# Kernel tuning notes

Measured on AMD Instinct MI355X. Metric: run time of the kernel, lower is better.

Reference implementation:

```python
import jax, jax.numpy as jnp
import numpy as np

L, D, B, N, H = 18, 256, 2, 1024, 4
HD = D // H  # head dim = 64
NAMES = ['self', 'cross'] * 9
BN_EPS = 1e-5


def conv1d(x, W, b):
    # pointwise Conv1d: x [B, Cin, N], W [Cout, Cin], b [Cout]
    return jnp.einsum('oi,bin->bon', W, x) + b[None, :, None]


def setup_inputs() -> dict:
    key = jax.random.key(0)
    ks = jax.random.split(key, 20)
    r = lambda k, shp, s=0.02: jax.random.normal(k, shp, dtype=jnp.float32) * s
    inp = {
        'desc0': jax.random.normal(ks[0], (B, D, N), dtype=jnp.float32),
        'desc1': jax.random.normal(ks[1], (B, D, N), dtype=jnp.float32),
        # attention projections (q, k, v, merge), stacked over layers
        'Wq': r(ks[2], (L, D, D)), 'bq': r(ks[3], (L, D)),
        'Wk': r(ks[4], (L, D, D)), 'bk': r(ks[5], (L, D)),
        'Wv': r(ks[6], (L, D, D)), 'bv': r(ks[7], (L, D)),
        'Wm': r(ks[8], (L, D, D)), 'bm': r(ks[9], (L, D)),
        # MLP([2D, 2D, D]): conv1 + BN(eval) + relu + conv2
        'W1': r(ks[10], (L, 2 * D, 2 * D)), 'b1': r(ks[11], (L, 2 * D)),
        'gamma': 1.0 + r(ks[12], (L, 2 * D)), 'beta': r(ks[13], (L, 2 * D)),
        'mu': r(ks[14], (L, 2 * D), 0.1),
        'var': 0.5 + jax.random.uniform(ks[15], (L, 2 * D), dtype=jnp.float32),
        'W2': r(ks[16], (L, D, 2 * D)), 'b2': r(ks[17], (L, D)),
    }
    return inp


def reference(desc0, desc1, Wq, bq, Wk, bk, Wv, bv, Wm, bm,
              W1, b1, gamma, beta, mu, var, W2, b2):
    d0, d1 = desc0, desc1
    bs = d0.shape[0]
    out0, out1 = [], []
    for i, name in enumerate(NAMES):
        x = jnp.concatenate([d0, d1], axis=0)           # [2B, D, N]
        src = x if name == 'self' else jnp.concatenate([d1, d0], axis=0)
        # QKV projections, split D -> (head_dim, H) matching torch .view(B, dim, H, -1)
        q = conv1d(x, Wq[i], bq[i]).reshape(2 * bs, HD, H, N)
        k = conv1d(src, Wk[i], bk[i]).reshape(2 * bs, HD, H, N)
        v = conv1d(src, Wv[i], bv[i]).reshape(2 * bs, HD, H, N)
        scores = jnp.einsum('bdhn,bdhm->bhnm', q, k) / np.sqrt(HD).astype(np.float32)
        prob = jax.nn.softmax(scores, axis=-1)          # [2B, H, N, N]
        att = jnp.einsum('bhnm,bdhm->bdhn', prob, v).reshape(2 * bs, D, N)
        message = conv1d(att, Wm[i], bm[i])             # merge
        y = jnp.concatenate([x, message], axis=1)       # [2B, 2D, N]
        h = conv1d(y, W1[i], b1[i])
        h = gamma[i][None, :, None] * (h - mu[i][None, :, None]) \
            * jax.lax.rsqrt(var[i][None, :, None] + BN_EPS) + beta[i][None, :, None]
        h = jax.nn.relu(h)
        delta = conv1d(h, W2[i], b2[i])                 # [2B, D, N]
        d0 = d0 + delta[:bs]
        d1 = d1 + delta[bs:]
        if name == 'cross':
            out0.append(d0)
            out1.append(d1)
    # [2, n_cross, B, D, N]
    return jnp.stack([jnp.stack(out0), jnp.stack(out1)])
```

## Files before the change

### kernel.cpp

```cpp
#include <hip/hip_runtime.h>
#include <math.h>


typedef unsigned short u16;
typedef unsigned int u32;
typedef __attribute__((ext_vector_type(4))) unsigned int u32x4;
typedef __attribute__((ext_vector_type(2))) unsigned int u32x2;
typedef __attribute__((ext_vector_type(8))) short short8v;
typedef __attribute__((ext_vector_type(4))) float f32x4;

union AB { u32x4 q; u32x2 d[2]; short8v s; };

__device__ __forceinline__ u16 f2bf(float f) {
  u32 u = __builtin_bit_cast(u32, f);
  u32 r = u + 0x7fffu + ((u >> 16) & 1u);
  return (u16)(r >> 16);
}

typedef const __attribute__((address_space(1))) void gas_t;
typedef __attribute__((address_space(3))) void las_t;
__device__ __forceinline__ void gld16(const void* g, void* l) {
  __builtin_amdgcn_global_load_lds((gas_t*)g, (las_t*)l, 16, 0, 0);
}
template<int NN>
__device__ __forceinline__ void waitvm() {
  if constexpr (NN == 0) asm volatile("s_waitcnt vmcnt(0)" ::: "memory");
  else if constexpr (NN == 1) asm volatile("s_waitcnt vmcnt(1)" ::: "memory");
  else if constexpr (NN == 2) asm volatile("s_waitcnt vmcnt(2)" ::: "memory");
  else if constexpr (NN == 3) asm volatile("s_waitcnt vmcnt(3)" ::: "memory");
  else asm volatile("s_waitcnt vmcnt(4)" ::: "memory");
}

template<int SN, int NK>
__device__ __forceinline__ void mm16g(const u16* __restrict__ Ar,
                                      const u16* const (&Br)[SN], f32x4 (&acc)[SN]) {
#pragma unroll
  for (int s = 0; s < SN; ++s) acc[s] = (f32x4){0.f, 0.f, 0.f, 0.f};
  AB a[2], b[2][SN];
  a[0].q = *(const u32x4*)(Ar);
#pragma unroll
  for (int s = 0; s < SN; ++s) b[0][s].q = *(const u32x4*)(Br[s]);
#pragma unroll
  for (int kp = 0; kp < NK; ++kp) {
    const int cu = kp & 1, nx = cu ^ 1;
    if (kp + 1 < NK) {
      a[nx].q = *(const u32x4*)(Ar + (kp + 1) * 32);
#pragma unroll
      for (int s = 0; s < SN; ++s) b[nx][s].q = *(const u32x4*)(Br[s] + (kp + 1) * 32);
    }
#pragma unroll
    for (int s = 0; s < SN; ++s)
      acc[s] = __builtin_amdgcn_mfma_f32_16x16x32_bf16(a[cu].s, b[cu][s].s, acc[s], 0, 0, 0);
  }
}

template<int LDB, int SN, int NS, int D>
__device__ __forceinline__ void mmlds(const u16* __restrict__ W, char* __restrict__ Wb,
                                      const char* __restrict__ Alds, f32x4 (&acc)[SN],
                                      int w, int lane, int l4, int l15, int R) {
  constexpr int NBUF = D + 1;
  constexpr int WREG = NBUF * SN * 1024;
  const int xj = (lane & 3) ^ ((lane >> 2) & 3) ^ ((lane >> 4) & 3);
  const int swzr = ((l15 & 3) ^ ((l15 >> 2) & 3)) << 4;
  const u16* gs = W + (size_t)(w * SN * 16 + (lane >> 2)) * LDB + xj * 8;
  char* ldsw = Wb + w * WREG;
#pragma unroll
  for (int s = 0; s < SN; ++s) acc[s] = (f32x4){0.f, 0.f, 0.f, 0.f};
#pragma unroll
  for (int d = 0; d < D; ++d) {
    const int sl = (R + d) & (NS - 1);
#pragma unroll
    for (int c = 0; c < SN; ++c)
      gld16(gs + (size_t)c * 16 * LDB + (size_t)sl * 32,
            ldsw + d * (SN * 1024) + c * 1024);
  }
#pragma unroll
  for (int i = 0; i < NS; ++i) {
    const int rem = NS - 1 - i;
    constexpr int DM1 = D - 1;
    if (rem >= DM1) waitvm<SN * DM1>();
    else if (rem == 2) waitvm<SN * 2>();
    else if (rem == 1) waitvm<SN>();
    else waitvm<0>();
    const int s = (i + R) & (NS - 1);
    const char* rb = ldsw + (i % NBUF) * (SN * 1024);
    AB af;
    af.q = *(const u32x4*)(Alds + ((l15 * 1024 + s * 64 + l4 * 16) ^ ((l15 & 7) << 4)));
#pragma unroll
    for (int t = 0; t < SN; ++t) {
      AB bf;
      bf.q = *(const u32x4*)(rb + t * 1024 + l15 * 64 + ((l4 << 4) ^ swzr));
      acc[t] = __builtin_amdgcn_mfma_f32_16x16x32_bf16(af.s, bf.s, acc[t], 0, 0, 0);
    }
    if (i + D < NS) {
      const int sl = (i + D + R) & (NS - 1);
#pragma unroll
      for (int c = 0; c < SN; ++c)
        gld16(gs + (size_t)c * 16 * LDB + (size_t)sl * 32,
              ldsw + ((i + D) % NBUF) * (SN * 1024) + c * 1024);
    }
  }
}

__global__ void k_setup(const float* __restrict__ Wq, const float* __restrict__ Wk,
                        const float* __restrict__ Wv, const float* __restrict__ Wm,
                        const float* __restrict__ W1, const float* __restrict__ W2,
                        const float* __restrict__ g, const float* __restrict__ be,
                        const float* __restrict__ mu, const float* __restrict__ va,
                        const float* __restrict__ b1, u16* __restrict__ wbf,
                        float* __restrict__ sc, float* __restrict__ sh) {
  int bid = blockIdx.x, tid = threadIdx.x;
  if (bid < 4608) {
    int which = bid / 1152, lb = bid - which * 1152;
    size_t i4 = ((size_t)lb * 256 + tid) * 4;
    int layer = (int)(i4 >> 16), rem = (int)(i4 & 65535);
    int row = rem >> 8, kk = rem & 255;
    const float* src = which == 0 ? Wq : which == 1 ? Wk : which == 2 ? Wv : Wm;
    f32x4 a = *(const f32x4*)(src + i4);
    u16* dl = wbf + (size_t)layer * 655360 + which * 65536;
    if (which < 3) {
      float s = (which == 0) ? 0.125f : 1.0f;
      int rp = ((row & 3) << 6) | (row >> 2);
      u32x2 pk;
      pk[0] = (u32)f2bf(a[0] * s) | ((u32)f2bf(a[1] * s) << 16);
      pk[1] = (u32)f2bf(a[2] * s) | ((u32)f2bf(a[3] * s) << 16);
      *(u32x2*)(dl + rp * 256 + kk) = pk;
    } else {
#pragma unroll
      for (int e = 0; e < 4; ++e) {
        int ci = kk + e, cp = ((ci & 3) << 6) | (ci >> 2);
        dl[row * 256 + cp] = f2bf(a[e]);
      }
    }
  } else if (bid < 9216) {
    int lb = bid - 4608;
    size_t i4 = ((size_t)lb * 256 + tid) * 4;
    int layer = (int)(i4 >> 18);
    size_t rem = i4 & 262143;
    f32x4 a = *(const f32x4*)(W1 + i4);
    u32x2 pk;
    pk[0] = (u32)f2bf(a[0]) | ((u32)f2bf(a[1]) << 16);
    pk[1] = (u32)f2bf(a[2]) | ((u32)f2bf(a[3]) << 16);
    *(u32x2*)(wbf + (size_t)layer * 655360 + 262144 + rem) = pk;
  } else if (bid < 11520) {
    int lb = bid - 9216;
    size_t i4 = ((size_t)lb * 256 + tid) * 4;
    int layer = (int)(i4 >> 17);
    size_t rem = i4 & 131071;
    f32x4 a = *(const f32x4*)(W2 + i4);
    u32x2 pk;
    pk[0] = (u32)f2bf(a[0]) | ((u32)f2bf(a[1]) << 16);
    pk[1] = (u32)f2bf(a[2]) | ((u32)f2bf(a[3]) << 16);
    *(u32x2*)(wbf + (size_t)layer * 655360 + 524288 + rem) = pk;
  } else {
    int i = (bid - 11520) * 256 + tid;
    if (i < 9216) {
      float s = g[i] * rsqrtf(va[i] + 1e-5f);
      sc[i] = s;
      sh[i] = s * (b1[i] - mu[i]) + be[i];
    }
  }
}

__global__ __launch_bounds__(256) void k_init(const float* __restrict__ d0,
                                              const float* __restrict__ d1,
                                              float* __restrict__ dstate,
                                              u16* __restrict__ y) {
  __shared__ float T[64 * 65];
  int b = blockIdx.z, cb = blockIdx.y * 64, nb = blockIdx.x * 64;
  int t = threadIdx.x, th = t >> 4, tl = t & 15;
  const float* src = (b < 2 ? d0 : d1) + (size_t)(b & 1) * 262144;
#pragma unroll
  for (int it = 0; it < 4; ++it) {
    int cl = it * 16 + th;
    f32x4 v = *(const f32x4*)(src + (size_t)(cb + cl) * 1024 + nb + tl * 4);
#pragma unroll
    for (int e = 0; e < 4; ++e) T[cl * 65 + tl * 4 + e] = v[e];
  }
  __syncthreads();
#pragma unroll
  for (int it = 0; it < 4; ++it) {
    int nl = it * 16 + th;
    f32x4 o;
#pragma unroll
    for (int e = 0; e < 4; ++e) o[e] = T[(tl * 4 + e) * 65 + nl];
    *(f32x4*)(dstate + (size_t)b * 262144 + (size_t)(nb + nl) * 256 + cb + tl * 4) = o;
    u32x2 pk;
    pk[0] = (u32)f2bf(o[0]) | ((u32)f2bf(o[1]) << 16);
    pk[1] = (u32)f2bf(o[2]) | ((u32)f2bf(o[3]) << 16);
    *(u32x2*)(y + (size_t)b * 524288 + (size_t)(nb + nl) * 512 + cb + tl * 4) = pk;
  }
}

__global__ __launch_bounds__(512) void k_qkv0(const u16* __restrict__ y,
                                              const u16* __restrict__ wln,
                                              const float* __restrict__ bqn,
                                              const float* __restrict__ bkn,
                                              const float* __restrict__ bvn,
                                              u16* __restrict__ qb, u16* __restrict__ kb,
                                              u16* __restrict__ vb) {
  const int row0 = blockIdx.x * 16, b = row0 >> 10, nb0 = row0 & 1023;
  const int tid = threadIdx.x, w = tid >> 6, lane = tid & 63;
  const int l4 = lane >> 4, l15 = lane & 15;
  const u16* Ar = y + (size_t)(row0 + l15) * 512 + l4 * 8;
  const u16* Br[6];
  f32x4 acc[6];
  int ty[6], cc[6];
#pragma unroll
  for (int s = 0; s < 6; ++s) {
    int gc = w * 96 + s * 16;
    ty[s] = gc >> 8;
    cc[s] = gc & 255;
    Br[s] = wln + ty[s] * 65536 + (size_t)(cc[s] + l15) * 256 + l4 * 8;
  }
  mm16g<6, 8>(Ar, Br, acc);
#pragma unroll
  for (int s = 0; s < 6; ++s) {
    int c = cc[s] + l15;
    int borig = ((c & 63) << 2) | (c >> 6);
    if (ty[s] == 0) {
      float bb = 0.125f * bqn[borig];
#pragma unroll
      for (int r = 0; r < 4; ++r)
        qb[(size_t)b * 262144 + (size_t)(nb0 + l4 * 4 + r) * 256 + c] = f2bf(acc[s][r] + bb);
    } else if (ty[s] == 1) {
      float bb = bkn[borig];
#pragma unroll
      for (int r = 0; r < 4; ++r)
        kb[(size_t)b * 262144 + (size_t)(nb0 + l4 * 4 + r) * 256 + c] = f2bf(acc[s][r] + bb);
    } else {
      float bb = bvn[borig];
      u32x2 pk;
      pk[0] = (u32)f2bf(acc[s][0] + bb) | ((u32)f2bf(acc[s][1] + bb) << 16);
      pk[1] = (u32)f2bf(acc[s][2] + bb) | ((u32)f2bf(acc[s][3] + bb) << 16);
      *(u32x2*)(vb + (size_t)b * 262144 + (size_t)c * 1024 + nb0 + l4 * 4) = pk;
    }
  }
}

__global__ __launch_bounds__(512) void k_attn(const u16* __restrict__ qbuf,
                                              const u16* __restrict__ kbuf,
                                              const u16* __restrict__ vbuf,
                                              u16* __restrict__ att, int crossmask) {
  __shared__ char Kt[2][2][8192];
  __shared__ char Vt[2][2][8192];
  __shared__ char Ps[8][2304];
  __shared__ float Ms[4][16], Ls[4][16], Os[4][16][68];
  const int nb = blockIdx.x * 64;
  const int bh = blockIdx.y, b = bh >> 2, h = bh & 3;
  const int srcb = b ^ crossmask;
  const int tid = threadIdx.x, w = tid >> 6, lane = tid & 63;
  const int l4 = lane >> 4, l15 = lane & 15;
  const int qt = w & 3, half = w >> 2;
  char* P = Ps[w];
  const u16* Qb = qbuf + (size_t)b * 262144 + h * 64;
  const u16* Kb = kbuf + (size_t)srcb * 262144 + h * 64;
  const u16* Vb = vbuf + (size_t)srcb * 262144 + (size_t)h * 65536;
  const int srow = tid >> 3, sj = (tid & 7) * 16, sx = sj ^ ((srow & 7) << 4);
  const u16* gK[2] = {Kb, Kb + 512 * 256};
  const u16* gV[2] = {Vb, Vb + 512};

  const int qrow = nb + qt * 16;
  AB qf[2];
#pragma unroll
  for (int ks = 0; ks < 2; ++ks)
    qf[ks].q = *(const u32x4*)(Qb + (size_t)(qrow + l15) * 256 + ks * 32 + l4 * 8);

  u32x4 sk[2], sv[2];
#pragma unroll
  for (int H = 0; H < 2; ++H) {
    sk[H] = *(const u32x4*)((const char*)(gK[H] + (size_t)srow * 256) + sj);
    sv[H] = *(const u32x4*)((const char*)(gV[H] + (size_t)srow * 1024) + sj);
  }
#pragma unroll
  for (int H = 0; H < 2; ++H) {
    *(u32x4*)(Kt[H][0] + srow * 128 + sx) = sk[H];
    *(u32x4*)(Vt[H][0] + srow * 128 + sx) = sv[H];
  }
  __syncthreads();

  f32x4 oacc[4];
#pragma unroll
  for (int s = 0; s < 4; ++s) oacc[s] = (f32x4){0.f, 0.f, 0.f, 0.f};
  float mst = -1e30f, lst = 0.f;

#pragma unroll
  for (int mt = 0; mt < 8; ++mt) {
    const int cur = mt & 1, nx = cur ^ 1;
    if (mt < 7) {
#pragma unroll
      for (int H = 0; H < 2; ++H) {
        sk[H] = *(const u32x4*)((const char*)(gK[H] + (size_t)((mt + 1) * 64 + srow) * 256) + sj);
        sv[H] = *(const u32x4*)((const char*)(gV[H] + (size_t)srow * 1024 + (mt + 1) * 64) + sj);
      }
    }
    f32x4 sa[4];
#pragma unroll
    for (int sm = 0; sm < 4; ++sm) {
      sa[sm] = (f32x4){0.f, 0.f, 0.f, 0.f};
#pragma unroll
      for (int ks = 0; ks < 2; ++ks) {
        AB kf;
        int rr = sm * 16 + l15;
        kf.q = *(const u32x4*)(Kt[half][cur] + rr * 128 + ((ks * 64 + l4 * 16) ^ ((rr & 7) << 4)));
        sa[sm] = __builtin_amdgcn_mfma_f32_16x16x32_bf16(kf.s, qf[ks].s, sa[sm], 0, 0, 0);
      }
    }
    float m1 = fmaxf(fmaxf(fmaxf(sa[0][0], sa[0][1]), fmaxf(sa[0][2], sa[0][3])),
                     fmaxf(fmaxf(sa[1][0], sa[1][1]), fmaxf(sa[1][2], sa[1][3])));
    float m2 = fmaxf(fmaxf(fmaxf(sa[2][0], sa[2][1]), fmaxf(sa[2][2], sa[2][3])),
                     fmaxf(fmaxf(sa[3][0], sa[3][1]), fmaxf(sa[3][2], sa[3][3])));
    m1 = fmaxf(m1, m2);
    m1 = fmaxf(m1, __shfl_xor(m1, 16));
    m1 = fmaxf(m1, __shfl_xor(m1, 32));
    float mnew = fmaxf(mst, m1);
    float corr = __expf(mst - mnew);
    mst = mnew;
    float rs = 0.f;
#pragma unroll
    for (int sm = 0; sm < 4; ++sm)
#pragma unroll
      for (int r = 0; r < 4; ++r) {
        float p = __expf(sa[sm][r] - mnew);
        sa[sm][r] = p;
        rs += p;
      }
    rs += __shfl_xor(rs, 16);
    rs += __shfl_xor(rs, 32);
    lst = lst * corr + rs;
#pragma unroll
    for (int r = 0; r < 4; ++r) {
      float cr = __shfl(corr, l4 * 4 + r);
#pragma unroll
      for (int s = 0; s < 4; ++s) oacc[s][r] *= cr;
    }
#pragma unroll
    for (int sm = 0; sm < 4; ++sm) {
      u32x2 pk;
      pk[0] = (u32)f2bf(sa[sm][0]) | ((u32)f2bf(sa[sm][1]) << 16);
      pk[1] = (u32)f2bf(sa[sm][2]) | ((u32)f2bf(sa[sm][3]) << 16);
      *(u32x2*)(P + l15 * 136 + (sm * 16 + l4 * 4) * 2) = pk;
    }
#pragma unroll
    for (int ks = 0; ks < 2; ++ks) {
      AB pf;
      const char* ra = P + l15 * 136 + ks * 64 + l4 * 16;
      pf.d[0] = *(const u32x2*)ra;
      pf.d[1] = *(const u32x2*)(ra + 8);
#pragma unroll
      for (int s = 0; s < 4; ++s) {
        AB vf;
        int rr = s * 16 + l15;
        vf.q = *(const u32x4*)(Vt[half][cur] + rr * 128 + ((ks * 64 + l4 * 16) ^ ((rr & 7) << 4)));
        oacc[s] = __builtin_amdgcn_mfma_f32_16x16x32_bf16(pf.s, vf.s, oacc[s], 0, 0, 0);
      }
    }
    if (mt < 7) {
#pragma unroll
      for (int H = 0; H < 2; ++H) {
        *(u32x4*)(Kt[H][nx] + srow * 128 + sx) = sk[H];
        *(u32x4*)(Vt[H][nx] + srow * 128 + sx) = sv[H];
      }
    }
    __syncthreads();
  }
  if (half == 1) {
    Ms[qt][l15] = mst;
    Ls[qt][l15] = lst;
#pragma unroll
    for (int s = 0; s < 4; ++s)
#pragma unroll
      for (int r = 0; r < 4; ++r) Os[qt][l4 * 4 + r][s * 16 + l15] = oacc[s][r];
  }
  __syncthreads();
  if (half == 0) {
    float mb = Ms[qt][l15], lb = Ls[qt][l15];
    float M = fmaxf(mst, mb);
    float ea = __expf(mst - M), eb = __expf(mb - M);
    float rl = 1.f / (lst * ea + lb * eb);
    float fa = ea * rl, fb = eb * rl;
#pragma unroll
    for (int r = 0; r < 4; ++r) {
      float far = __shfl(fa, l4 * 4 + r);
      float fbr = __shfl(fb, l4 * 4 + r);
      int n = nb + qt * 16 + l4 * 4 + r;
#pragma unroll
      for (int s = 0; s < 4; ++s) {
        float ov = oacc[s][r] * far + Os[qt][l4 * 4 + r][s * 16 + l15] * fbr;
        att[(size_t)b * 262144 + (size_t)n * 256 + h * 64 + s * 16 + l15] = f2bf(ov);
      }
    }
  }
}

__global__ __launch_bounds__(1024) void k_post(
    const u16* __restrict__ att, const u16* __restrict__ wl, const u16* __restrict__ wln,
    const float* __restrict__ bm, const float* __restrict__ sc, const float* __restrict__ sh,
    const float* __restrict__ b2, const float* __restrict__ bqn,
    const float* __restrict__ bkn, const float* __restrict__ bvn,
    float* __restrict__ dstate, u16* __restrict__ y, u16* __restrict__ qb,
    u16* __restrict__ kb, u16* __restrict__ vb, float* __restrict__ out, int cross, int j,
    int last) {
  __shared__ char yT[16384];
  __shared__ char hT[16384];
  __shared__ char Wb[98304];
  const int bid = blockIdx.x;
  const int row0 = bid * 16, b = row0 >> 10, nb0 = row0 & 1023;
  const int tid = threadIdx.x, w = tid >> 6, lane = tid & 63;
  const int l4 = lane >> 4, l15 = lane & 15;

  {
    int rr = tid >> 6, ch = tid & 63;
    u32x4 v = *(const u32x4*)(y + (size_t)(row0 + rr) * 512 + ch * 8);
    *(u32x4*)(yT + ((rr * 1024 + ch * 16) ^ ((rr & 7) << 4))) = v;
    if (tid < 512) {
      int ra = tid >> 5, ca = tid & 31;
      u32x4 va = *(const u32x4*)(att + (size_t)(row0 + ra) * 256 + ca * 8);
      *(u32x4*)(hT + ((ra * 1024 + ca * 16) ^ ((ra & 7) << 4))) = va;
    }
  }
  __syncthreads();
  {
    f32x4 acc[1];
    mmlds<256, 1, 8, 3>(wl + 196608, Wb, hT, acc, w, lane, l4, l15, bid & 7);
    int c = w * 16 + l15;
    float bb = bm[c];
#pragma unroll
    for (int r = 0; r < 4; ++r) {
      int rw = l4 * 4 + r;
      *(u16*)(yT + ((rw * 1024 + (256 + c) * 2) ^ ((rw & 7) << 4))) = f2bf(acc[0][r] + bb);
    }
  }
  __syncthreads();
  {
    f32x4 acc[2];
    mmlds<512, 2, 16, 2>(wl + 262144, Wb, yT, acc, w, lane, l4, l15, bid & 15);
#pragma unroll
    for (int s = 0; s < 2; ++s) {
      int c = w * 32 + s * 16 + l15;
      float s_ = sc[c], t_ = sh[c];
#pragma unroll
      for (int r = 0; r < 4; ++r) {
        int rw = l4 * 4 + r;
        *(u16*)(hT + ((rw * 1024 + c * 2) ^ ((rw & 7) << 4))) =
            f2bf(fmaxf(s_ * acc[s][r] + t_, 0.f));
      }
    }
  }
  __syncthreads();
  {
    f32x4 acc[1];
    mmlds<512, 1, 16, 3>(wl + 524288, Wb, hT, acc, w, lane, l4, l15, bid & 15);
    float* ob = out + (size_t)(((b >> 1) * 9 + j) * 2 + (b & 1)) * 262144;
    int c = w * 16 + l15;
    float bb = b2[c];
#pragma unroll
    for (int r = 0; r < 4; ++r) {
      int rw = l4 * 4 + r;
      size_t di = (size_t)(row0 + rw) * 256 + c;
      float nv = dstate[di] + acc[0][r] + bb;
      dstate[di] = nv;
      u16 bv16 = f2bf(nv);
      y[(size_t)(row0 + rw) * 512 + c] = bv16;
      *(u16*)(yT + ((rw * 1024 + c * 2) ^ ((rw & 7) << 4))) = bv16;
      if (cross) ob[(size_t)c * 1024 + nb0 + rw] = nv;
    }
  }
  if (last) return;
  __syncthreads();
  {
    f32x4 acc[2];
    mmlds<256, 2, 8, 2>(wln, Wb, yT, acc, w, lane, l4, l15, bid & 7);
#pragma unroll
    for (int s = 0; s < 2; ++s) {
      int gc = w * 32 + s * 16;
      int ty = gc >> 8;
      int c = (gc & 255) + l15;
      int borig = ((c & 63) << 2) | (c >> 6);
      if (ty == 0) {
        float bb = 0.125f * bqn[borig];
#pragma unroll
        for (int r = 0; r < 4; ++r)
          qb[(size_t)b * 262144 + (size_t)(nb0 + l4 * 4 + r) * 256 + c] = f2bf(acc[s][r] + bb);
      } else {
        float bb = bkn[borig];
#pragma unroll
        for (int r = 0; r < 4; ++r)
          kb[(size_t)b * 262144 + (size_t)(nb0 + l4 * 4 + r) * 256 + c] = f2bf(acc[s][r] + bb);
      }
    }
  }
  __syncthreads();
  {
    f32x4 acc[1];
    mmlds<256, 1, 8, 3>(wln + 131072, Wb, yT, acc, w, lane, l4, l15, bid & 7);
    int c = w * 16 + l15;
    float bb = bvn[((c & 63) << 2) | (c >> 6)];
    u32x2 pk;
    pk[0] = (u32)f2bf(acc[0][0] + bb) | ((u32)f2bf(acc[0][1] + bb) << 16);
    pk[1] = (u32)f2bf(acc[0][2] + bb) | ((u32)f2bf(acc[0][3] + bb) << 16);
    *(u32x2*)(vb + (size_t)b * 262144 + (size_t)c * 1024 + nb0 + l4 * 4) = pk;
  }
}

extern "C" void kernel_launch(void* const* d_in, const int* in_sizes, int n_in,
                              void* d_out, int out_size, void* d_ws, size_t ws_size,
                              hipStream_t stream) {
  const float* desc0 = (const float*)d_in[0];
  const float* desc1 = (const float*)d_in[1];
  const float* Wq = (const float*)d_in[2];
  const float* bq = (const float*)d_in[3];
  const float* Wk = (const float*)d_in[4];
  const float* bk = (const float*)d_in[5];
  const float* Wv = (const float*)d_in[6];
  const float* bv = (const float*)d_in[7];
  const float* Wm = (const float*)d_in[8];
  const float* bm = (const float*)d_in[9];
  const float* W1 = (const float*)d_in[10];
  const float* b1 = (const float*)d_in[11];
  const float* gamma = (const float*)d_in[12];
  const float* beta = (const float*)d_in[13];
  const float* mu = (const float*)d_in[14];
  const float* var = (const float*)d_in[15];
  const float* W2 = (const float*)d_in[16];
  const float* b2 = (const float*)d_in[17];

  char* ws = (char*)d_ws;
  float* dstate = (float*)ws;
  u16* y = (u16*)(ws + ((size_t)4 << 20));
  u16* qb = (u16*)(ws + ((size_t)8 << 20));
  u16* kb = (u16*)(ws + ((size_t)10 << 20));
  u16* vb = (u16*)(ws + ((size_t)12 << 20));
  u16* attb = (u16*)(ws + ((size_t)14 << 20));
  u16* wbf = (u16*)(ws + ((size_t)16 << 20));
  float* scb = (float*)(ws + ((size_t)40 << 20));
  float* shb = (float*)(ws + ((size_t)41 << 20));

  k_setup<<<11556, 256, 0, stream>>>(Wq, Wk, Wv, Wm, W1, W2, gamma, beta, mu, var, b1,
                                     wbf, scb, shb);
  k_init<<<dim3(16, 4, 4), 256, 0, stream>>>(desc0, desc1, dstate, y);
  k_qkv0<<<256, 512, 0, stream>>>(y, wbf, bq, bk, bv, qb, kb, vb);

  for (int i = 0; i < 18; ++i) {
    int cross = i & 1;
    const u16* wl = wbf + (size_t)i * 655360;
    int nl = (i < 17) ? i + 1 : 0;
    const u16* wln = wbf + (size_t)nl * 655360;
    k_attn<<<dim3(16, 16), 512, 0, stream>>>(qb, kb, vb, attb, cross ? 2 : 0);
    k_post<<<256, 1024, 0, stream>>>(attb, wl, wln, bm + i * 256, scb + (size_t)i * 512,
                                     shb + (size_t)i * 512, b2 + i * 256, bq + nl * 256,
                                     bk + nl * 256, bv + nl * 256, dstate, y, qb, kb, vb,
                                     (float*)d_out, cross, i >> 1, i == 17);
  }
}
```

Baseline: 735.9 us.

## Restructure k_post weight streaming into per-wave single-tile deep prefetch ring

```diff
diff --git a/kernel.cpp b/kernel.cpp
--- a/kernel.cpp
+++ b/kernel.cpp
@@ -28,7 +28,8 @@
   else if constexpr (NN == 1) asm volatile("s_waitcnt vmcnt(1)" ::: "memory");
   else if constexpr (NN == 2) asm volatile("s_waitcnt vmcnt(2)" ::: "memory");
   else if constexpr (NN == 3) asm volatile("s_waitcnt vmcnt(3)" ::: "memory");
-  else asm volatile("s_waitcnt vmcnt(4)" ::: "memory");
+  else if constexpr (NN == 4) asm volatile("s_waitcnt vmcnt(4)" ::: "memory");
+  else asm volatile("s_waitcnt vmcnt(5)" ::: "memory");
 }
 
 template<int SN, int NK>
@@ -54,50 +55,39 @@
   }
 }
 
-template<int LDB, int SN, int NS, int D>
-__device__ __forceinline__ void mmlds(const u16* __restrict__ W, char* __restrict__ Wb,
-                                      const char* __restrict__ Alds, f32x4 (&acc)[SN],
-                                      int w, int lane, int l4, int l15, int R) {
-  constexpr int NBUF = D + 1;
-  constexpr int WREG = NBUF * SN * 1024;
+template<int LDB, int NS, int D>
+__device__ __forceinline__ void mmw(const u16* __restrict__ Wcol, char* __restrict__ ldsw,
+                                    const char* __restrict__ Alds, f32x4& acc0,
+                                    int lane, int l4, int l15, int R) {
+  constexpr int DI = D < NS ? D : NS;
+  constexpr int NBUF = DI + 1;
   const int xj = (lane & 3) ^ ((lane >> 2) & 3) ^ ((lane >> 4) & 3);
   const int swzr = ((l15 & 3) ^ ((l15 >> 2) & 3)) << 4;
-  const u16* gs = W + (size_t)(w * SN * 16 + (lane >> 2)) * LDB + xj * 8;
-  char* ldsw = Wb + w * WREG;
-#pragma unroll
-  for (int s = 0; s < SN; ++s) acc[s] = (f32x4){0.f, 0.f, 0.f, 0.f};
-#pragma unroll
-  for (int d = 0; d < D; ++d) {
+  const u16* gs = Wcol + (size_t)(lane >> 2) * LDB + xj * 8;
+  acc0 = (f32x4){0.f, 0.f, 0.f, 0.f};
+#pragma unroll
+  for (int d = 0; d < DI; ++d) {
     const int sl = (R + d) & (NS - 1);
-#pragma unroll
-    for (int c = 0; c < SN; ++c)
-      gld16(gs + (size_t)c * 16 * LDB + (size_t)sl * 32,
-            ldsw + d * (SN * 1024) + c * 1024);
+    gld16(gs + (size_t)sl * 32, ldsw + d * 1024);
   }
 #pragma unroll
   for (int i = 0; i < NS; ++i) {
     const int rem = NS - 1 - i;
-    constexpr int DM1 = D - 1;
-    if (rem >= DM1) waitvm<SN * DM1>();
-    else if (rem == 2) waitvm<SN * 2>();
-    else if (rem == 1) waitvm<SN>();
+    if (rem >= DI - 1) waitvm<DI - 1>();
+    else if (rem == 4) waitvm<4>();
+    else if (rem == 3) waitvm<3>();
+    else if (rem == 2) waitvm<2>();
+    else if (rem == 1) waitvm<1>();
     else waitvm<0>();
     const int s = (i + R) & (NS - 1);
-    const char* rb = ldsw + (i % NBUF) * (SN * 1024);
-    AB af;
+    const char* rb = ldsw + (i % NBUF) * 1024;
+    AB af, bf;
     af.q = *(const u32x4*)(Alds + ((l15 * 1024 + s * 64 + l4 * 16) ^ ((l15 & 7) << 4)));
-#pragma unroll
-    for (int t = 0; t < SN; ++t) {
-      AB bf;
-      bf.q = *(const u32x4*)(rb + t * 1024 + l15 * 64 + ((l4 << 4) ^ swzr));
-      acc[t] = __builtin_amdgcn_mfma_f32_16x16x32_bf16(af.s, bf.s, acc[t], 0, 0, 0);
-    }
-    if (i + D < NS) {
-      const int sl = (i + D + R) & (NS - 1);
-#pragma unroll
-      for (int c = 0; c < SN; ++c)
-        gld16(gs + (size_t)c * 16 * LDB + (size_t)sl * 32,
-              ldsw + ((i + D) % NBUF) * (SN * 1024) + c * 1024);
+    bf.q = *(const u32x4*)(rb + l15 * 64 + ((l4 << 4) ^ swzr));
+    acc0 = __builtin_amdgcn_mfma_f32_16x16x32_bf16(af.s, bf.s, acc0, 0, 0, 0);
+    if (i + DI < NS) {
+      const int sl = (i + DI + R) & (NS - 1);
+      gld16(gs + (size_t)sl * 32, ldsw + ((i + DI) % NBUF) * 1024);
     }
   }
 }
@@ -403,11 +393,12 @@
     int last) {
   __shared__ char yT[16384];
   __shared__ char hT[16384];
-  __shared__ char Wb[98304];
+  __shared__ char Wb[114688];
   const int bid = blockIdx.x;
   const int row0 = bid * 16, b = row0 >> 10, nb0 = row0 & 1023;
   const int tid = threadIdx.x, w = tid >> 6, lane = tid & 63;
   const int l4 = lane >> 4, l15 = lane & 15;
+  char* ring = Wb + w * 7168;
 
   {
     int rr = tid >> 6, ch = tid & 63;
@@ -421,36 +412,40 @@
   }
   __syncthreads();
   {
-    f32x4 acc[1];
-    mmlds<256, 1, 8, 3>(wl + 196608, Wb, hT, acc, w, lane, l4, l15, bid & 7);
+    f32x4 acc;
+    mmw<256, 8, 6>(wl + 196608 + (size_t)(w * 16) * 256, ring, hT, acc, lane, l4, l15,
+                   bid & 7);
     int c = w * 16 + l15;
     float bb = bm[c];
 #pragma unroll
     for (int r = 0; r < 4; ++r) {
       int rw = l4 * 4 + r;
-      *(u16*)(yT + ((rw * 1024 + (256 + c) * 2) ^ ((rw & 7) << 4))) = f2bf(acc[0][r] + bb);
+      *(u16*)(yT + ((rw * 1024 + (256 + c) * 2) ^ ((rw & 7) << 4))) = f2bf(acc[r] + bb);
     }
   }
   __syncthreads();
   {
-    f32x4 acc[2];
-    mmlds<512, 2, 16, 2>(wl + 262144, Wb, yT, acc, w, lane, l4, l15, bid & 15);
-#pragma unroll
-    for (int s = 0; s < 2; ++s) {
-      int c = w * 32 + s * 16 + l15;
+#pragma unroll
+    for (int p = 0; p < 2; ++p) {
+      f32x4 acc;
+      const int colbase = p * 256 + w * 16;
+      mmw<512, 16, 6>(wl + 262144 + (size_t)colbase * 512, ring, yT, acc, lane, l4, l15,
+                      (bid + p * 5) & 15);
+      int c = colbase + l15;
       float s_ = sc[c], t_ = sh[c];
 #pragma unroll
       for (int r = 0; r < 4; ++r) {
         int rw = l4 * 4 + r;
         *(u16*)(hT + ((rw * 1024 + c * 2) ^ ((rw & 7) << 4))) =
-            f2bf(fmaxf(s_ * acc[s][r] + t_, 0.f));
+            f2bf(fmaxf(s_ * acc[r] + t_, 0.f));
       }
     }
   }
   __syncthreads();
   {
-    f32x4 acc[1];
-    mmlds<512, 1, 16, 3>(wl + 524288, Wb, hT, acc, w, lane, l4, l15, bid & 15);
+    f32x4 acc;
+    mmw<512, 16, 6>(wl + 524288 + (size_t)(w * 16) * 512, ring, hT, acc, lane, l4, l15,
+                    bid & 15);
     float* ob = out + (size_t)(((b >> 1) * 9 + j) * 2 + (b & 1)) * 262144;
     int c = w * 16 + l15;
     float bb = b2[c];
@@ -458,7 +453,7 @@
     for (int r = 0; r < 4; ++r) {
       int rw = l4 * 4 + r;
       size_t di = (size_t)(row0 + rw) * 256 + c;
-      float nv = dstate[di] + acc[0][r] + bb;
+      float nv = dstate[di] + acc[r] + bb;
       dstate[di] = nv;
       u16 bv16 = f2bf(nv);
       y[(size_t)(row0 + rw) * 512 + c] = bv16;
@@ -469,37 +464,31 @@
   if (last) return;
   __syncthreads();
   {
-    f32x4 acc[2];
-    mmlds<256, 2, 8, 2>(wln, Wb, yT, acc, w, lane, l4, l15, bid & 7);
-#pragma unroll
-    for (int s = 0; s < 2; ++s) {
-      int gc = w * 32 + s * 16;
-      int ty = gc >> 8;
-      int c = (gc & 255) + l15;
+#pragma unroll
+    for (int p = 0; p < 3; ++p) {
+      f32x4 acc;
+      mmw<256, 8, 6>(wln + p * 65536 + (size_t)(w * 16) * 256, ring, yT, acc, lane, l4,
+                     l15, (bid + p * 3) & 7);
+      int c = w * 16 + l15;
       int borig = ((c & 63) << 2) | (c >> 6);
-      if (ty == 0) {
+      if (p == 0) {
         float bb = 0.125f * bqn[borig];
 #pragma unroll
         for (int r = 0; r < 4; ++r)
-          qb[(size_t)b * 262144 + (size_t)(nb0 + l4 * 4 + r) * 256 + c] = f2bf(acc[s][r] + bb);
+          qb[(size_t)b * 262144 + (size_t)(nb0 + l4 * 4 + r) * 256 + c] = f2bf(acc[r] + bb);
+      } else if (p == 1) {
+        float bb = bkn[borig];
+#pragma unroll
+        for (int r = 0; r < 4; ++r)
+          kb[(size_t)b * 262144 + (size_t)(nb0 + l4 * 4 + r) * 256 + c] = f2bf(acc[r] + bb);
       } else {
-        float bb = bkn[borig];
-#pragma unroll
-        for (int r = 0; r < 4; ++r)
-          kb[(size_t)b * 262144 + (size_t)(nb0 + l4 * 4 + r) * 256 + c] = f2bf(acc[s][r] + bb);
-      }
-    }
-  }
-  __syncthreads();
-  {
-    f32x4 acc[1];
-    mmlds<256, 1, 8, 3>(wln + 131072, Wb, yT, acc, w, lane, l4, l15, bid & 7);
-    int c = w * 16 + l15;
-    float bb = bvn[((c & 63) << 2) | (c >> 6)];
-    u32x2 pk;
-    pk[0] = (u32)f2bf(acc[0][0] + bb) | ((u32)f2bf(acc[0][1] + bb) << 16);
-    pk[1] = (u32)f2bf(acc[0][2] + bb) | ((u32)f2bf(acc[0][3] + bb) << 16);
-    *(u32x2*)(vb + (size_t)b * 262144 + (size_t)c * 1024 + nb0 + l4 * 4) = pk;
+        float bb = bvn[borig];
+        u32x2 pk;
+        pk[0] = (u32)f2bf(acc[0] + bb) | ((u32)f2bf(acc[1] + bb) << 16);
+        pk[1] = (u32)f2bf(acc[2] + bb) | ((u32)f2bf(acc[3] + bb) << 16);
+        *(u32x2*)(vb + (size_t)b * 262144 + (size_t)c * 1024 + nb0 + l4 * 4) = pk;
+      }
+    }
   }
 }
 
```

After: 693.7 us (median of 2 runs). -5.7%, faster.
